# Kernel optimization log

Measured on AMD Instinct MI355X. Metric: run time of the kernel, lower is better.

The kernel has to match this reference:

```python
import jax, jax.numpy as jnp
import numpy as np

B = 8          # batch of images
FH = FW = 28   # feature map size (layer2 of wide_resnet101_2 on 224x224)
IMG = 224      # input image H=W
C = 1024       # embedding dim (max of layer2/layer3 channels)
M = 50000      # coreset memory bank size
KS = 17        # GaussianBlur kernel size
SIGMA = 4.0


def _gauss_kernel():
    x = jnp.arange(KS, dtype=jnp.float32) - (KS - 1) / 2.0
    g = jnp.exp(-(x * x) / (2.0 * SIGMA * SIGMA))
    return g / jnp.sum(g)


def _gaussian_blur(masks):
    # masks: [B, H, W]; separable depthwise blur with reflect padding
    k = _gauss_kernel()
    pad = (KS - 1) // 2
    x = jnp.pad(masks, ((0, 0), (pad, pad), (pad, pad)), mode='reflect')[:, None]  # [B,1,H+2p,W+2p]
    x = jax.lax.conv_general_dilated(x, k[None, None, :, None], (1, 1), 'VALID',
                                     dimension_numbers=('NCHW', 'OIHW', 'NCHW'))
    x = jax.lax.conv_general_dilated(x, k[None, None, None, :], (1, 1), 'VALID',
                                     dimension_numbers=('NCHW', 'OIHW', 'NCHW'))
    return x[:, 0]


def setup_inputs() -> dict:
    key = jax.random.key(0)
    k1, k2 = jax.random.split(key)
    features = jax.random.normal(k1, (B * FH * FW, C), dtype=jnp.float32)
    memory = jax.random.normal(k2, (M, C), dtype=jnp.float32)
    return {"features": features, "memory": memory}


def reference(features, memory):
    # pairwise squared L2 distances via ||f||^2 + ||m||^2 - 2 f.m  -> [N, M]
    f2 = jnp.sum(features * features, axis=-1)            # [N]
    m2 = jnp.sum(memory * memory, axis=-1)                # [M]
    d2 = f2[:, None] + m2[None, :] - 2.0 * (features @ memory.T)
    score = jnp.sqrt(jnp.maximum(jnp.min(d2, axis=-1), 0.0))  # [N]
    image_scores = jnp.max(score.reshape(B, -1), axis=-1)     # [B]
    masks = score.reshape(B, FH, FW)
    # bilinear, align_corners=False == jax.image.resize 'linear' (half-pixel centers)
    masks = jax.image.resize(masks, (B, IMG, IMG), method='linear')
    masks = _gaussian_blur(masks)
    return image_scores, masks
```

## Files before the change

### kernel.cpp

```cpp
#include <hip/hip_runtime.h>
#include <hip/hip_bf16.h>
#include <float.h>

#define N_FEAT 6272
#define C_DIM  1024
#define M_MEM  50000
#define M_PAD  50048
#define B_IMG  8
#define IMGSZ  224
#define NTILES_M 49
#define NTILES_N 391
#define NTILES   19159
#define PER_XCD  2395
#define GRID_PAD 19160

typedef __attribute__((ext_vector_type(8))) short bf16x8;
typedef __attribute__((ext_vector_type(4))) float f32x4;


__device__ inline unsigned short f2bf(float x) {
  unsigned int u = __float_as_uint(x);
  u += 0x7FFFu + ((u >> 16) & 1u);
  return (unsigned short)(u >> 16);
}

__global__ __launch_bounds__(256) void convert_rows_kernel(
    const float* __restrict__ src, unsigned short* __restrict__ dst,
    float* __restrict__ sq, unsigned int* __restrict__ minbits,
    int valid_rows, int total_rows)
{
  int row  = blockIdx.x * 4 + (threadIdx.x >> 6);
  int lane = threadIdx.x & 63;
  if (row >= total_rows) return;
  float s = 0.f;
  ushort4* d4 = (ushort4*)(dst + (size_t)row * C_DIM);
  if (row < valid_rows) {
    const float4* s4 = (const float4*)(src + (size_t)row * C_DIM);
    #pragma unroll
    for (int j = 0; j < 4; ++j) {
      float4 v = s4[lane + 64 * j];
      ushort4 o = make_ushort4(f2bf(v.x), f2bf(v.y), f2bf(v.z), f2bf(v.w));
      d4[lane + 64 * j] = o;
      s += v.x * v.x + v.y * v.y + v.z * v.z + v.w * v.w;
    }
  } else {
    ushort4 z = make_ushort4(0, 0, 0, 0);
    #pragma unroll
    for (int j = 0; j < 4; ++j) d4[lane + 64 * j] = z;
  }
  #pragma unroll
  for (int off = 32; off > 0; off >>= 1) s += __shfl_down(s, off, 64);
  if (lane == 0) {
    sq[row] = (row < valid_rows) ? s : FLT_MAX;
    if (minbits && row < valid_rows) minbits[row] = 0x7F7FFFFFu;
  }
}

__global__ __launch_bounds__(256, 3) void gemm_min_kernel(
    const unsigned short* __restrict__ A,
    const unsigned short* __restrict__ Bm,
    const float* __restrict__ f2, const float* __restrict__ m2,
    unsigned int* __restrict__ minbits)
{
  __shared__ unsigned short lA[2][4096];
  __shared__ unsigned short lB[2][4096];

  const int lid = blockIdx.x;
  const int t = (lid & 7) * PER_XCD + (lid >> 3);
  if (t >= NTILES) return;
  const int tileN = t / NTILES_M;
  const int tileM = t - tileN * NTILES_M;

  const int tid  = threadIdx.x;
  const int wave = tid >> 6, lane = tid & 63;
  const int wr = wave >> 1, wc = wave & 1;
  const int quad = lane >> 4, r16 = lane & 15;

  f32x4 acc[4][4] = {};

  const int q    = tid & 3;
  const int rowS = tid >> 2;
  const unsigned short* gA = A  + (size_t)(tileM * 128 + rowS) * C_DIM + q * 8;
  const unsigned short* gB = Bm + (size_t)(tileN * 128 + rowS) * C_DIM + q * 8;
  const int g1 = 64 * C_DIM;
  const int wOff0 = (q * 128 + (rowS        ^ (q << 1))) * 8;
  const int wOff1 = (q * 128 + ((rowS + 64) ^ (q << 1))) * 8;

  const int aidx = quad * 128 + wr * 64 + (r16 ^ (quad << 1));
  const int bidx = quad * 128 + wc * 64 + (r16 ^ (quad << 1));

  int4 pA0, pA1, pB0, pB1;

  pA0 = *(const int4*)(gA);
  pA1 = *(const int4*)(gA + g1);
  pB0 = *(const int4*)(gB);
  pB1 = *(const int4*)(gB + g1);
  *(int4*)(&lA[0][wOff0]) = pA0;
  *(int4*)(&lA[0][wOff1]) = pA1;
  *(int4*)(&lB[0][wOff0]) = pB0;
  *(int4*)(&lB[0][wOff1]) = pB1;
  pA0 = *(const int4*)(gA + 32);
  pA1 = *(const int4*)(gA + g1 + 32);
  pB0 = *(const int4*)(gB + 32);
  pB1 = *(const int4*)(gB + g1 + 32);
  __syncthreads();

  auto step = [&](int pbuf, int kt, bool doLoad) {
    const bf16x8* LA_ = (const bf16x8*)lA[pbuf];
    const bf16x8* LB_ = (const bf16x8*)lB[pbuf];
    bf16x8 a[4], b[4];
    #pragma unroll
    for (int i = 0; i < 4; ++i) a[i] = LA_[aidx + i * 16];
    #pragma unroll
    for (int j = 0; j < 4; ++j) b[j] = LB_[bidx + j * 16];
    #pragma unroll
    for (int i = 0; i < 4; ++i)
      #pragma unroll
      for (int j = 0; j < 4; ++j)
        acc[i][j] = __builtin_amdgcn_mfma_f32_16x16x32_bf16(a[i], b[j], acc[i][j], 0, 0, 0);
    __syncthreads();
    unsigned short* wA = lA[pbuf ^ 1];
    unsigned short* wB = lB[pbuf ^ 1];
    *(int4*)(wA + wOff0) = pA0;
    *(int4*)(wA + wOff1) = pA1;
    *(int4*)(wB + wOff0) = pB0;
    *(int4*)(wB + wOff1) = pB1;
    if (doLoad) {
      const int o = (kt + 2) * 32;
      pA0 = *(const int4*)(gA + o);
      pA1 = *(const int4*)(gA + g1 + o);
      pB0 = *(const int4*)(gB + o);
      pB1 = *(const int4*)(gB + g1 + o);
    }
    __syncthreads();
  };

  for (int kt = 0; kt < 30; kt += 2) {
    step(0, kt, true);
    step(1, kt + 1, true);
  }
  step(0, 30, false);
  step(1, 31, false);

  const int colbase = tileN * 128 + wc * 64 + r16;
  float m2v[4];
  #pragma unroll
  for (int u = 0; u < 4; ++u) m2v[u] = m2[colbase + u * 16];
  const int rowq = tileM * 128 + wr * 64 + quad * 4;
  #pragma unroll
  for (int i = 0; i < 4; ++i) {
    #pragma unroll
    for (int r = 0; r < 4; ++r) {
      int n = rowq + i * 16 + r;
      float f2v = f2[n];
      float best = FLT_MAX;
      #pragma unroll
      for (int u = 0; u < 4; ++u) {
        float d = f2v + m2v[u] - 2.0f * acc[i][u][r];
        d = fmaxf(d, 0.0f);
        best = fminf(best, d);
      }
      best = fminf(best, __shfl_xor(best, 1, 64));
      best = fminf(best, __shfl_xor(best, 2, 64));
      best = fminf(best, __shfl_xor(best, 4, 64));
      best = fminf(best, __shfl_xor(best, 8, 64));
      if (r16 == 0) atomicMin(minbits + n, __float_as_uint(best));
    }
  }
}

__global__ __launch_bounds__(256) void finalize_kernel(
    const unsigned int* __restrict__ minbits, float* __restrict__ m28,
    float* __restrict__ image_scores)
{
  int b = blockIdx.x, tid = threadIdx.x;
  float mx = 0.f;
  for (int i = tid; i < 784; i += 256) {
    float s = sqrtf(__uint_as_float(minbits[b * 784 + i]));
    m28[b * 784 + i] = s;
    mx = fmaxf(mx, s);
  }
  #pragma unroll
  for (int off = 32; off > 0; off >>= 1) mx = fmaxf(mx, __shfl_down(mx, off, 64));
  __shared__ float red[4];
  if ((tid & 63) == 0) red[tid >> 6] = mx;
  __syncthreads();
  if (tid == 0) image_scores[b] = fmaxf(fmaxf(red[0], red[1]), fmaxf(red[2], red[3]));
}

__global__ __launch_bounds__(256) void resize_kernel(
    const float* __restrict__ m28, float* __restrict__ out)
{
  int idx = blockIdx.x * 256 + threadIdx.x;
  if (idx >= B_IMG * IMGSZ * IMGSZ) return;
  int x = idx % IMGSZ, y = (idx / IMGSZ) % IMGSZ, b = idx / (IMGSZ * IMGSZ);
  float sy = (y + 0.5f) * 0.125f - 0.5f;
  float sx = (x + 0.5f) * 0.125f - 0.5f;
  int iy0 = (int)floorf(sy); float fy = sy - (float)iy0;
  int ix0 = (int)floorf(sx); float fx = sx - (float)ix0;
  int y0 = min(max(iy0, 0), 27), y1 = min(max(iy0 + 1, 0), 27);
  int x0 = min(max(ix0, 0), 27), x1 = min(max(ix0 + 1, 0), 27);
  const float* p = m28 + b * 784;
  float v00 = p[y0 * 28 + x0], v01 = p[y0 * 28 + x1];
  float v10 = p[y1 * 28 + x0], v11 = p[y1 * 28 + x1];
  out[idx] = (1.f - fy) * ((1.f - fx) * v00 + fx * v01) +
             fy         * ((1.f - fx) * v10 + fx * v11);
}

__device__ inline void gauss17(float* g) {
  float s = 0.f;
  #pragma unroll
  for (int i = 0; i < 17; ++i) {
    float x = (float)(i - 8);
    g[i] = expf(-x * x * (1.0f / 32.0f));
    s += g[i];
  }
  float inv = 1.0f / s;
  #pragma unroll
  for (int i = 0; i < 17; ++i) g[i] *= inv;
}

__device__ inline int refl(int t) { return t < 0 ? -t : (t > 223 ? 446 - t : t); }

__global__ __launch_bounds__(256) void blur_h_kernel(
    const float* __restrict__ in, float* __restrict__ out)
{
  int idx = blockIdx.x * 256 + threadIdx.x;
  if (idx >= B_IMG * IMGSZ * IMGSZ) return;
  int x = idx % IMGSZ, y = (idx / IMGSZ) % IMGSZ, b = idx / (IMGSZ * IMGSZ);
  float g[17]; gauss17(g);
  const float* row = in + (size_t)b * IMGSZ * IMGSZ + y * IMGSZ;
  float s = 0.f;
  #pragma unroll
  for (int k = 0; k < 17; ++k) s += g[k] * row[refl(x + k - 8)];
  out[idx] = s;
}

__global__ __launch_bounds__(256) void blur_v_kernel(
    const float* __restrict__ in, float* __restrict__ out)
{
  int idx = blockIdx.x * 256 + threadIdx.x;
  if (idx >= B_IMG * IMGSZ * IMGSZ) return;
  int x = idx % IMGSZ, y = (idx / IMGSZ) % IMGSZ, b = idx / (IMGSZ * IMGSZ);
  float g[17]; gauss17(g);
  const float* img = in + (size_t)b * IMGSZ * IMGSZ;
  float s = 0.f;
  #pragma unroll
  for (int k = 0; k < 17; ++k) s += g[k] * img[refl(y + k - 8) * IMGSZ + x];
  out[idx] = s;
}

extern "C" void kernel_launch(void* const* d_in, const int* in_sizes, int n_in,
                              void* d_out, int out_size, void* d_ws, size_t ws_size,
                              hipStream_t stream) {
  const float* features = (const float*)d_in[0];
  const float* memory   = (const float*)d_in[1];
  if (n_in >= 2 && in_sizes[0] > in_sizes[1]) {
    const float* t = features; features = memory; memory = t;
  }
  float* out = (float*)d_out;
  char* ws = (char*)d_ws;

  unsigned short* memB  = (unsigned short*)(ws);
  unsigned short* featB = (unsigned short*)(ws + 102498304);
  float*        f2      = (float*)(ws + 115343360);
  float*        m2      = (float*)(ws + 115368448);
  unsigned int* minb    = (unsigned int*)(ws + 115568640);
  float*        m28     = (float*)(ws + 115593728);
  float*        rsz     = (float*)(ws + 115618816);
  float*        tmp     = (float*)(ws + 117224448);

  convert_rows_kernel<<<M_PAD / 4, 256, 0, stream>>>(memory, memB, m2, nullptr, M_MEM, M_PAD);
  convert_rows_kernel<<<N_FEAT / 4, 256, 0, stream>>>(features, featB, f2, minb, N_FEAT, N_FEAT);

  gemm_min_kernel<<<GRID_PAD, 256, 0, stream>>>(featB, memB, f2, m2, minb);

  finalize_kernel<<<B_IMG, 256, 0, stream>>>(minb, m28, out);
  resize_kernel<<<(B_IMG * IMGSZ * IMGSZ) / 256, 256, 0, stream>>>(m28, rsz);
  blur_h_kernel<<<(B_IMG * IMGSZ * IMGSZ) / 256, 256, 0, stream>>>(rsz, tmp);
  blur_v_kernel<<<(B_IMG * IMGSZ * IMGSZ) / 256, 256, 0, stream>>>(tmp, out + 8);
}
```

Measured before the change: 1.126 ms.

## Rewrite GEMM-min with 256x256 tiles and 4-stage direct global-to-LDS pipeline

Enlarges the GEMM tile from 128x128 to 256x256 with 512-thread blocks, so each block covers more output per staged byte. Global loads now go straight to LDS through global_load_lds into a 4-stage ring buffer, with explicit vmcnt waits and a single barrier per k-step. It also raises MFMA priority with s_setprio and groups tiles per XCD for better L2 locality. In exchange it uses 128KB of dynamic LDS, pads features and memory to 256-row multiples, and reuses workspace for the blur buffers.

```diff
diff --git a/kernel.cpp b/kernel.cpp
--- a/kernel.cpp
+++ b/kernel.cpp
@@ -3,16 +3,15 @@
 #include <float.h>
 
 #define N_FEAT 6272
+#define N_FPAD 6400
 #define C_DIM  1024
 #define M_MEM  50000
-#define M_PAD  50048
+#define M_PAD  50176
 #define B_IMG  8
 #define IMGSZ  224
-#define NTILES_M 49
-#define NTILES_N 391
-#define NTILES   19159
-#define PER_XCD  2395
-#define GRID_PAD 19160
+#define NTM    25
+#define NTN    196
+#define NT     4900
 
 typedef __attribute__((ext_vector_type(8))) short bf16x8;
 typedef __attribute__((ext_vector_type(4))) float f32x4;
@@ -56,107 +55,105 @@
   }
 }
 
-__global__ __launch_bounds__(256, 3) void gemm_min_kernel(
+__global__ __launch_bounds__(512, 2) void gemm_min_kernel(
     const unsigned short* __restrict__ A,
     const unsigned short* __restrict__ Bm,
     const float* __restrict__ f2, const float* __restrict__ m2,
     unsigned int* __restrict__ minbits)
 {
-  __shared__ unsigned short lA[2][4096];
-  __shared__ unsigned short lB[2][4096];
-
-  const int lid = blockIdx.x;
-  const int t = (lid & 7) * PER_XCD + (lid >> 3);
-  if (t >= NTILES) return;
-  const int tileN = t / NTILES_M;
-  const int tileM = t - tileN * NTILES_M;
+  extern __shared__ char smem[];
+
+  const int orig = blockIdx.x;
+  const int xcd  = orig & 7;
+  const int wg   = ((xcd < 4) ? xcd * 613 : 2452 + (xcd - 4) * 612) + (orig >> 3);
+  const int g    = wg / 980;
+  const int rem  = wg - g * 980;
+  const int tileN = rem / 5;
+  const int tileM = g * 5 + (rem - tileN * 5);
 
   const int tid  = threadIdx.x;
-  const int wave = tid >> 6, lane = tid & 63;
-  const int wr = wave >> 1, wc = wave & 1;
+  const int w    = tid >> 6, lane = tid & 63;
+  const int wr   = w >> 2, wc = w & 3;
   const int quad = lane >> 4, r16 = lane & 15;
 
-  f32x4 acc[4][4] = {};
-
-  const int q    = tid & 3;
-  const int rowS = tid >> 2;
-  const unsigned short* gA = A  + (size_t)(tileM * 128 + rowS) * C_DIM + q * 8;
-  const unsigned short* gB = Bm + (size_t)(tileN * 128 + rowS) * C_DIM + q * 8;
-  const int g1 = 64 * C_DIM;
-  const int wOff0 = (q * 128 + (rowS        ^ (q << 1))) * 8;
-  const int wOff1 = (q * 128 + ((rowS + 64) ^ (q << 1))) * 8;
-
-  const int aidx = quad * 128 + wr * 64 + (r16 ^ (quad << 1));
-  const int bidx = quad * 128 + wc * 64 + (r16 ^ (quad << 1));
-
-  int4 pA0, pA1, pB0, pB1;
-
-  pA0 = *(const int4*)(gA);
-  pA1 = *(const int4*)(gA + g1);
-  pB0 = *(const int4*)(gB);
-  pB1 = *(const int4*)(gB + g1);
-  *(int4*)(&lA[0][wOff0]) = pA0;
-  *(int4*)(&lA[0][wOff1]) = pA1;
-  *(int4*)(&lB[0][wOff0]) = pB0;
-  *(int4*)(&lB[0][wOff1]) = pB1;
-  pA0 = *(const int4*)(gA + 32);
-  pA1 = *(const int4*)(gA + g1 + 32);
-  pB0 = *(const int4*)(gB + 32);
-  pB1 = *(const int4*)(gB + g1 + 32);
-  __syncthreads();
-
-  auto step = [&](int pbuf, int kt, bool doLoad) {
-    const bf16x8* LA_ = (const bf16x8*)lA[pbuf];
-    const bf16x8* LB_ = (const bf16x8*)lB[pbuf];
-    bf16x8 a[4], b[4];
-    #pragma unroll
-    for (int i = 0; i < 4; ++i) a[i] = LA_[aidx + i * 16];
-    #pragma unroll
-    for (int j = 0; j < 4; ++j) b[j] = LB_[bidx + j * 16];
-    #pragma unroll
-    for (int i = 0; i < 4; ++i)
+  const unsigned short* gA[2];
+  const unsigned short* gB[2];
+  int offA[2], offB[2];
+  #pragma unroll
+  for (int j = 0; j < 2; ++j) {
+    const int m = w * 2 + j;
+    const int q = m >> 2;
+    const int row = ((m & 3) * 64 + lane) ^ q;
+    gA[j] = A  + (size_t)(tileM * 256 + row) * C_DIM + q * 8;
+    gB[j] = Bm + (size_t)(tileN * 256 + row) * C_DIM + q * 8;
+    offA[j] = m * 1024;
+    offB[j] = 16384 + m * 1024;
+  }
+
+  auto stage = [&](int kt) {
+    char* sl = smem + ((kt & 3) << 15);
+    const int ko = kt * 32;
+    #pragma unroll
+    for (int j = 0; j < 2; ++j) {
+      __builtin_amdgcn_global_load_lds(
+        (const __attribute__((address_space(1))) unsigned int*)(gA[j] + ko),
+        (__attribute__((address_space(3))) unsigned int*)(sl + offA[j]), 16, 0, 0);
+      __builtin_amdgcn_global_load_lds(
+        (const __attribute__((address_space(1))) unsigned int*)(gB[j] + ko),
+        (__attribute__((address_space(3))) unsigned int*)(sl + offB[j]), 16, 0, 0);
+    }
+  };
+
+  f32x4 acc[8][4] = {};
+  const int aIdx0 = quad * 256 + wr * 128 + (r16 ^ quad);
+  const int bIdx0 = quad * 256 + wc * 64  + (r16 ^ quad);
+
+  stage(0); stage(1); stage(2);
+
+  auto body = [&](int kt, bool doStage) {
+    __builtin_amdgcn_s_barrier();
+    __builtin_amdgcn_sched_barrier(0);
+    const bf16x8* LA = (const bf16x8*)(smem + ((kt & 3) << 15));
+    const bf16x8* LB = (const bf16x8*)(smem + ((kt & 3) << 15) + 16384);
+    bf16x8 a[8], b[4];
+    #pragma unroll
+    for (int i = 0; i < 8; ++i) a[i] = LA[aIdx0 + i * 16];
+    #pragma unroll
+    for (int j = 0; j < 4; ++j) b[j] = LB[bIdx0 + j * 16];
+    if (doStage) stage(kt + 3);
+    __builtin_amdgcn_s_setprio(1);
+    #pragma unroll
+    for (int i = 0; i < 8; ++i)
       #pragma unroll
       for (int j = 0; j < 4; ++j)
         acc[i][j] = __builtin_amdgcn_mfma_f32_16x16x32_bf16(a[i], b[j], acc[i][j], 0, 0, 0);
-    __syncthreads();
-    unsigned short* wA = lA[pbuf ^ 1];
-    unsigned short* wB = lB[pbuf ^ 1];
-    *(int4*)(wA + wOff0) = pA0;
-    *(int4*)(wA + wOff1) = pA1;
-    *(int4*)(wB + wOff0) = pB0;
-    *(int4*)(wB + wOff1) = pB1;
-    if (doLoad) {
-      const int o = (kt + 2) * 32;
-      pA0 = *(const int4*)(gA + o);
-      pA1 = *(const int4*)(gA + g1 + o);
-      pB0 = *(const int4*)(gB + o);
-      pB1 = *(const int4*)(gB + g1 + o);
-    }
-    __syncthreads();
+    __builtin_amdgcn_s_setprio(0);
   };
 
-  for (int kt = 0; kt < 30; kt += 2) {
-    step(0, kt, true);
-    step(1, kt + 1, true);
-  }
-  step(0, 30, false);
-  step(1, 31, false);
-
-  const int colbase = tileN * 128 + wc * 64 + r16;
+  for (int kt = 0; kt < 30; ++kt) {
+    asm volatile("s_waitcnt vmcnt(8)" ::: "memory");
+    body(kt, kt < 29);
+  }
+  asm volatile("s_waitcnt vmcnt(4)" ::: "memory");
+  body(30, false);
+  asm volatile("s_waitcnt vmcnt(0)" ::: "memory");
+  body(31, false);
+
+  const int colbase = tileN * 256 + wc * 64 + r16;
   float m2v[4];
   #pragma unroll
-  for (int u = 0; u < 4; ++u) m2v[u] = m2[colbase + u * 16];
-  const int rowq = tileM * 128 + wr * 64 + quad * 4;
-  #pragma unroll
-  for (int i = 0; i < 4; ++i) {
+  for (int j = 0; j < 4; ++j) m2v[j] = m2[colbase + j * 16];
+  const int rowq = tileM * 256 + wr * 128 + quad * 4;
+  #pragma unroll
+  for (int i = 0; i < 8; ++i) {
     #pragma unroll
     for (int r = 0; r < 4; ++r) {
-      int n = rowq + i * 16 + r;
-      float f2v = f2[n];
+      const int n = rowq + i * 16 + r;
+      const float f2v = f2[n];
       float best = FLT_MAX;
       #pragma unroll
-      for (int u = 0; u < 4; ++u) {
-        float d = f2v + m2v[u] - 2.0f * acc[i][u][r];
+      for (int j = 0; j < 4; ++j) {
+        float d = f2v + m2v[j] - 2.0f * acc[i][j][r];
         d = fmaxf(d, 0.0f);
         best = fminf(best, d);
       }
@@ -262,18 +259,25 @@
   char* ws = (char*)d_ws;
 
   unsigned short* memB  = (unsigned short*)(ws);
-  unsigned short* featB = (unsigned short*)(ws + 102498304);
-  float*        f2      = (float*)(ws + 115343360);
-  float*        m2      = (float*)(ws + 115368448);
-  unsigned int* minb    = (unsigned int*)(ws + 115568640);
-  float*        m28     = (float*)(ws + 115593728);
-  float*        rsz     = (float*)(ws + 115618816);
-  float*        tmp     = (float*)(ws + 117224448);
+  unsigned short* featB = (unsigned short*)(ws + 102760448);
+  float*        f2      = (float*)(ws + 115867648);
+  float*        m2      = (float*)(ws + 115893248);
+  unsigned int* minb    = (unsigned int*)(ws + 116093952);
+  float*        m28     = (float*)(ws + 116119552);
+  float*        rsz     = (float*)(ws);
+  float*        tmp     = (float*)(ws + 1605632);
+
+  static int attr_done = 0;
+  if (!attr_done) {
+    hipFuncSetAttribute((const void*)gemm_min_kernel,
+                        hipFuncAttributeMaxDynamicSharedMemorySize, 131072);
+    attr_done = 1;
+  }
 
   convert_rows_kernel<<<M_PAD / 4, 256, 0, stream>>>(memory, memB, m2, nullptr, M_MEM, M_PAD);
-  convert_rows_kernel<<<N_FEAT / 4, 256, 0, stream>>>(features, featB, f2, minb, N_FEAT, N_FEAT);
-
-  gemm_min_kernel<<<GRID_PAD, 256, 0, stream>>>(featB, memB, f2, m2, minb);
+  convert_rows_kernel<<<N_FPAD / 4, 256, 0, stream>>>(features, featB, f2, minb, N_FEAT, N_FPAD);
+
+  gemm_min_kernel<<<NT, 512, 131072, stream>>>(featB, memB, f2, m2, minb);
 
   finalize_kernel<<<B_IMG, 256, 0, stream>>>(minb, m28, out);
   resize_kernel<<<(B_IMG * IMGSZ * IMGSZ) / 256, 256, 0, stream>>>(m28, rsz);
```

After: 1.545 ms. 1.37x slower.
